# Optimization experiments

Measured on AMD Instinct MI355X. Metric: run time of the kernel, lower is better.

Reference implementation:

```python
import jax, jax.numpy as jnp
import numpy as np

C = 192; G = 12; CG = C // G          # channels, groups, channels per group
KS = 3; PAD = 1; K = KS * KS - 1      # 3x3 kernel, remove_center=True -> 8 points
HID = 4 * C                           # mlp_ratio = 4
OFFSET_SCALE = 1.0

# kernel dilation grid (x, y) pairs, center removed (remove_center=True)
_pts = np.arange(KS) - (KS - 1) // 2
_gx, _gy = np.meshgrid(_pts, _pts, indexing='ij')
_grid = np.stack([_gx.ravel(), _gy.ravel()], -1).astype(np.float32)
_grid = _grid[~np.all(_grid == 0, axis=1)]   # (K, 2)
GRID = jnp.asarray(_grid)


def _ln(x, w, b, eps=1e-5):
    mu = jnp.mean(x, -1, keepdims=True)
    var = jnp.var(x, -1, keepdims=True)
    return (x - mu) * jax.lax.rsqrt(var + eps) * w + b


def _dcnv3(x, in_proj_w, in_proj_b, dw_w, dw_b, dw_ln_w, dw_ln_b,
           off_w, off_b, mask_w, mask_b, cfs_w, cfs_b, out_proj_w, out_proj_b):
    # x: (B, H, W, C) channels-last
    B, H, W, _ = x.shape
    xp = x @ in_proj_w + in_proj_b          # value / x_proj
    # depthwise conv -> LN -> GELU on the raw input (offset/mask branch)
    x1 = jax.lax.conv_general_dilated(
        x, dw_w, (1, 1), 'SAME',
        dimension_numbers=('NHWC', 'HWIO', 'NHWC'),
        feature_group_count=C) + dw_b
    x1 = jax.nn.gelu(_ln(x1, dw_ln_w, dw_ln_b, 1e-6), approximate=False)
    off = (x1 @ off_w + off_b).reshape(B, H, W, G, K, 2)      # (dx, dy) in pixels
    mask = jax.nn.softmax((x1 @ mask_w + mask_b).reshape(B, H, W, G, K), axis=-1)
    # pad value and flatten spatial; (B, Hp*Wp, G, 1, CG)
    Hp, Wp = H + 2 * PAD, W + 2 * PAD
    v = jnp.pad(xp, ((0, 0), (PAD, PAD), (PAD, PAD), (0, 0))).reshape(B, Hp * Wp, G, 1, CG)
    # sampling locations in padded-image pixel index coords (grid_sample align_corners=False)
    bx = jnp.arange(W, dtype=x.dtype)[None, None, :, None, None] + PAD
    by = jnp.arange(H, dtype=x.dtype)[None, :, None, None, None] + PAD
    px = (bx + (GRID[:, 0] + off[..., 0]) * OFFSET_SCALE).reshape(B, H * W, G, K)
    py = (by + (GRID[:, 1] + off[..., 1]) * OFFSET_SCALE).reshape(B, H * W, G, K)
    x0 = jnp.floor(px); y0 = jnp.floor(py)
    wx = px - x0; wy = py - y0
    ix0 = x0.astype(jnp.int32); iy0 = y0.astype(jnp.int32)

    def gather(iy, ix):
        valid = ((iy >= 0) & (iy < Hp) & (ix >= 0) & (ix < Wp)).astype(x.dtype)
        idx = jnp.clip(iy, 0, Hp - 1) * Wp + jnp.clip(ix, 0, Wp - 1)
        s = jnp.take_along_axis(v, idx[..., None], axis=1)    # (B, HW, G, K, CG)
        return s * valid[..., None]

    s = (gather(iy0, ix0)         * ((1 - wy) * (1 - wx))[..., None]
       + gather(iy0, ix0 + 1)     * ((1 - wy) * wx)[..., None]
       + gather(iy0 + 1, ix0)     * (wy * (1 - wx))[..., None]
       + gather(iy0 + 1, ix0 + 1) * (wy * wx)[..., None])
    out = jnp.einsum('bngk,bngkc->bngc', mask.reshape(B, H * W, G, K), s).reshape(B, H, W, C)
    # center feature scale
    cfs = jax.nn.sigmoid(x1 @ cfs_w.T + cfs_b)                # (B, H, W, G)
    cfs = jnp.repeat(cfs, CG, axis=-1)                        # (B, H, W, C)
    out = out * (1 - cfs) + xp * cfs
    return out @ out_proj_w + out_proj_b


def _forward(x, norm1_w, norm1_b, norm2_w, norm2_b, rpn1_w, rpn1_b, rpn2_w, rpn2_b,
             in_proj_w, in_proj_b, dw_w, dw_b, dw_ln_w, dw_ln_b, off_w, off_b,
             mask_w, mask_b, cfs_w, cfs_b, out_proj_w, out_proj_b,
             fc1_w, fc1_b, fc2_w, fc2_b):
    d = _dcnv3(_ln(x, norm1_w, norm1_b), in_proj_w, in_proj_b, dw_w, dw_b,
               dw_ln_w, dw_ln_b, off_w, off_b, mask_w, mask_b, cfs_w, cfs_b,
               out_proj_w, out_proj_b)
    x = x + _ln(d, rpn1_w, rpn1_b)                            # res_post_norm branch 1
    h = jax.nn.gelu(_ln(x, norm2_w, norm2_b) @ fc1_w + fc1_b, approximate=False) @ fc2_w + fc2_b
    x = x + _ln(h, rpn2_w, rpn2_b)                            # res_post_norm branch 2
    return x


def setup_inputs():
    key = jax.random.key(0)
    ks = jax.random.split(key, 12)
    r = lambda i, shape, s=0.02: jax.random.normal(ks[i], shape, jnp.float32) * s
    B, H, W = 4, 56, 56
    return dict(
        x=jax.random.normal(ks[0], (B, H, W, C), jnp.float32),
        norm1_w=jnp.ones((C,)), norm1_b=jnp.zeros((C,)),
        norm2_w=jnp.ones((C,)), norm2_b=jnp.zeros((C,)),
        rpn1_w=jnp.ones((C,)), rpn1_b=jnp.zeros((C,)),
        rpn2_w=jnp.ones((C,)), rpn2_b=jnp.zeros((C,)),
        in_proj_w=r(1, (C, C)), in_proj_b=jnp.zeros((C,)),
        dw_w=r(2, (KS, KS, 1, C), 0.1), dw_b=jnp.zeros((C,)),
        dw_ln_w=jnp.ones((C,)), dw_ln_b=jnp.zeros((C,)),
        off_w=r(3, (C, G * K * 2), 0.1), off_b=jnp.zeros((G * K * 2,)),
        mask_w=r(4, (C, G * K), 0.1), mask_b=jnp.zeros((G * K,)),
        cfs_w=r(5, (G, C), 0.1), cfs_b=jnp.zeros((G,)),
        out_proj_w=r(6, (C, C)), out_proj_b=jnp.zeros((C,)),
        fc1_w=r(7, (C, HID)), fc1_b=jnp.zeros((HID,)),
        fc2_w=r(8, (HID, C)), fc2_b=jnp.zeros((C,)),
    )


def reference(x, norm1_w, norm1_b, norm2_w, norm2_b, rpn1_w, rpn1_b, rpn2_w, rpn2_b,
              in_proj_w, in_proj_b, dw_w, dw_b, dw_ln_w, dw_ln_b, off_w, off_b,
              mask_w, mask_b, cfs_w, cfs_b, out_proj_w, out_proj_b,
              fc1_w, fc1_b, fc2_w, fc2_b):
    return _forward(x, norm1_w, norm1_b, norm2_w, norm2_b, rpn1_w, rpn1_b, rpn2_w, rpn2_b,
                    in_proj_w, in_proj_b, dw_w, dw_b, dw_ln_w, dw_ln_b, off_w, off_b,
                    mask_w, mask_b, cfs_w, cfs_b, out_proj_w, out_proj_b,
                    fc1_w, fc1_b, fc2_w, fc2_b)
```

## Files before the change

### kernel.cpp

```cpp
#include <hip/hip_runtime.h>
#include <hip/hip_bf16.h>
#include <math.h>


#define BATCH 4
#define HH 56
#define WW 56
#define CC 192
#define NPIX (BATCH * HH * WW)
#define XS_STR 200
#define H1S 776
#define OFS 193
#define MLS 97

typedef __hip_bfloat16 bf16;
typedef __attribute__((ext_vector_type(8))) short short8;
typedef __attribute__((ext_vector_type(4))) float float4v;

__device__ __forceinline__ float gelu_exact(float x) {
    return 0.5f * x * (1.f + erff(x * 0.70710678118654752f));
}
__device__ __forceinline__ bf16 f2b(float f) { return __float2bfloat16(f); }
__device__ __forceinline__ float b2f(bf16 h) { return __bfloat162float(h); }
__device__ __forceinline__ float4 ldb4(const bf16* p) {
    const ushort4 u = *(const ushort4*)p;
    float4 r;
    r.x = __uint_as_float((unsigned)u.x << 16);
    r.y = __uint_as_float((unsigned)u.y << 16);
    r.z = __uint_as_float((unsigned)u.z << 16);
    r.w = __uint_as_float((unsigned)u.w << 16);
    return r;
}
__device__ __forceinline__ void stb4(bf16* p, float4 v) {
    ushort4 u;
    bf16 h;
    h = f2b(v.x); u.x = *(unsigned short*)&h;
    h = f2b(v.y); u.y = *(unsigned short*)&h;
    h = f2b(v.z); u.z = *(unsigned short*)&h;
    h = f2b(v.w); u.w = *(unsigned short*)&h;
    *(ushort4*)p = u;
}

__global__ __launch_bounds__(256) void ln4_k(const float* __restrict__ X,
        const float* __restrict__ w, const float* __restrict__ b,
        bf16* __restrict__ out, float eps)
{
    const int pix  = blockIdx.x * 4 + (threadIdx.x >> 6);
    const int lane = threadIdx.x & 63;
    const size_t base = (size_t)pix * CC;
    float v[3];
    #pragma unroll
    for (int i = 0; i < 3; i++) v[i] = X[base + lane + 64 * i];
    float s = v[0] + v[1] + v[2];
    float q = v[0]*v[0] + v[1]*v[1] + v[2]*v[2];
    #pragma unroll
    for (int off = 32; off > 0; off >>= 1) {
        s += __shfl_xor(s, off, 64);
        q += __shfl_xor(q, off, 64);
    }
    const float mu  = s * (1.f / CC);
    const float var = q * (1.f / CC) - mu * mu;
    const float rs  = rsqrtf(var + eps);
    #pragma unroll
    for (int i = 0; i < 3; i++) {
        const int c = lane + 64 * i;
        out[base + c] = f2b((v[i] - mu) * rs * w[c] + b[c]);
    }
}

__global__ __launch_bounds__(256) void dwconv_ln_gelu_k(
        const bf16* __restrict__ xn, const float* __restrict__ dww,
        const float* __restrict__ dwb, const float* __restrict__ lnw,
        const float* __restrict__ lnb, bf16* __restrict__ x1)
{
    __shared__ float cv[4][192];
    const int bid  = (blockIdx.x & 7) * (NPIX / 32) + (blockIdx.x >> 3);
    const int t    = threadIdx.x;
    const int ws   = t >> 6;
    const int l    = t & 63;
    const int pix  = bid * 4 + ws;
    const int bimg = pix / (HH * WW);
    const int hw   = pix - bimg * HH * WW;
    const int h    = hw / WW;
    const int wx   = hw - h * WW;

    if (l < 48) {
        const int c0 = l * 4;
        float4 acc = *(const float4*)&dwb[c0];
        #pragma unroll
        for (int ky = 0; ky < 3; ky++) {
            const int yy = h + ky - 1;
            if (yy < 0 || yy >= HH) continue;
            #pragma unroll
            for (int kx = 0; kx < 3; kx++) {
                const int xx = wx + kx - 1;
                if (xx < 0 || xx >= WW) continue;
                const float4 a = ldb4(&xn[((size_t)(bimg * HH + yy) * WW + xx) * CC + c0]);
                const float4 ww = *(const float4*)&dww[(ky * 3 + kx) * CC + c0];
                acc.x += a.x * ww.x; acc.y += a.y * ww.y;
                acc.z += a.z * ww.z; acc.w += a.w * ww.w;
            }
        }
        *(float4*)&cv[ws][c0] = acc;
    }
    __syncthreads();

    float v[3];
    #pragma unroll
    for (int i = 0; i < 3; i++) v[i] = cv[ws][l + 64 * i];
    float s = v[0] + v[1] + v[2];
    float q = v[0]*v[0] + v[1]*v[1] + v[2]*v[2];
    #pragma unroll
    for (int off = 32; off > 0; off >>= 1) {
        s += __shfl_xor(s, off, 64);
        q += __shfl_xor(q, off, 64);
    }
    const float mu  = s * (1.f / CC);
    const float var = q * (1.f / CC) - mu * mu;
    const float rs  = rsqrtf(var + 1e-6f);
    #pragma unroll
    for (int i = 0; i < 3; i++) {
        const int c = l + 64 * i;
        x1[(size_t)pix * CC + c] = f2b(gelu_exact((v[i] - mu) * rs * lnw[c] + lnb[c]));
    }
}

__global__ __launch_bounds__(256) void prep_w_k(const float* __restrict__ inpw,
        const float* __restrict__ offw, const float* __restrict__ maskw,
        const float* __restrict__ outpw, const float* __restrict__ fc1w,
        const float* __restrict__ fc2w, bf16* __restrict__ wsB)
{
    const int i = blockIdx.x * 256 + threadIdx.x;
    bf16* inpP = wsB;
    bf16* omP  = wsB + 36864;
    bf16* outP = wsB + 92160;
    bf16* fc1P = wsB + 129024;
    bf16* fc2P = wsB + 276480;
    const int j   = i & 7;
    const int l   = (i >> 3) & 63;
    const int n15 = l & 15, q = l >> 4;
    const int grp = i >> 9;
    if (i < 36864) {
        const int t = grp / 6, c = grp - t * 6;
        const int n = 16 * t + n15, k = 32 * c + 8 * q + j;
        inpP[i] = f2b(inpw[(size_t)k * 192 + n]);
        outP[i] = f2b(outpw[(size_t)k * 192 + n]);
    }
    if (i < 55296) {
        const int t = grp / 6, c = grp - t * 6;
        const int n = 16 * t + n15, k = 32 * c + 8 * q + j;
        omP[i] = (n < 192) ? f2b(offw[(size_t)k * 192 + n])
                           : f2b(maskw[(size_t)k * 96 + (n - 192)]);
    }
    if (i < 147456) {
        const int t1 = grp / 6, c1 = grp - t1 * 6;
        const int n1 = 16 * t1 + n15, k1 = 32 * c1 + 8 * q + j;
        fc1P[i] = f2b(fc1w[(size_t)k1 * 768 + n1]);
        const int t2 = grp / 24, c2 = grp - t2 * 24;
        const int n2 = 16 * t2 + n15, k2 = 32 * c2 + 8 * q + j;
        fc2P[i] = f2b(fc2w[(size_t)k2 * 192 + n2]);
    }
}

__global__ __launch_bounds__(256) void gemm16_k(const bf16* __restrict__ A,
        const bf16* __restrict__ wP, const float* __restrict__ bias,
        bf16* __restrict__ out)
{
    __shared__ __align__(16) bf16 xs[16 * XS_STR];
    const int tid = threadIdx.x;
    const int w   = tid >> 6;
    const int l   = tid & 63;
    const int n15 = l & 15;
    const int q   = l >> 4;
    const int p0  = blockIdx.x * 16;

    for (int i = tid; i < 16 * 24; i += 256) {
        const int px = i / 24, c8 = i - px * 24;
        *(short8*)&xs[px * XS_STR + c8 * 8] = *(const short8*)&A[(size_t)(p0 + px) * 192 + c8 * 8];
    }
    __syncthreads();

    short8 aF[6];
    #pragma unroll
    for (int c = 0; c < 6; c++)
        aF[c] = *(const short8*)&xs[n15 * XS_STR + c * 32 + q * 8];

    #pragma unroll
    for (int t = 0; t < 3; t++) {
        const int tile = 3 * w + t;
        float4v acc = (float4v){0.f, 0.f, 0.f, 0.f};
        #pragma unroll
        for (int c = 0; c < 6; c++) {
            const short8 bF = *(const short8*)&wP[(size_t)((tile * 6 + c) * 64 + l) * 8];
            acc = __builtin_amdgcn_mfma_f32_16x16x32_bf16(aF[c], bF, acc, 0, 0, 0);
        }
        const int n0 = 16 * tile;
        const float bb = bias[n0 + n15];
        #pragma unroll
        for (int r = 0; r < 4; r++)
            out[(size_t)(p0 + 4 * q + r) * 192 + n0 + n15] = f2b(acc[r] + bb);
    }
}

__global__ __launch_bounds__(256) void offmask_sample_k(
        const bf16* __restrict__ xp, const bf16* __restrict__ x1g,
        const bf16* __restrict__ omP, const float* __restrict__ offb,
        const float* __restrict__ maskb, const float* __restrict__ cfsw,
        const float* __restrict__ cfsb, bf16* __restrict__ outb)
{
    __shared__ __align__(16) bf16 xs[16 * XS_STR];
    __shared__ float offs_l[16][OFS];
    __shared__ float mls_l[16][MLS];

    const int tid = threadIdx.x;
    const int w   = tid >> 6;
    const int l   = tid & 63;
    const int n15 = l & 15;
    const int q   = l >> 4;
    const int bid = (blockIdx.x & 7) * (NPIX / 128) + (blockIdx.x >> 3);
    const int p0  = bid * 16;

    for (int i = tid; i < 16 * 24; i += 256) {
        const int px = i / 24, c8 = i - px * 24;
        *(short8*)&xs[px * XS_STR + c8 * 8] = *(const short8*)&x1g[(size_t)(p0 + px) * 192 + c8 * 8];
    }
    __syncthreads();

    {
        short8 aF[6];
        #pragma unroll
        for (int c = 0; c < 6; c++)
            aF[c] = *(const short8*)&xs[n15 * XS_STR + c * 32 + q * 8];

        for (int t = w; t < 18; t += 4) {
            float4v acc = (float4v){0.f, 0.f, 0.f, 0.f};
            #pragma unroll
            for (int c = 0; c < 6; c++) {
                const short8 bF = *(const short8*)&omP[(size_t)((t * 6 + c) * 64 + l) * 8];
                acc = __builtin_amdgcn_mfma_f32_16x16x32_bf16(aF[c], bF, acc, 0, 0, 0);
            }
            const int n0 = 16 * t;
            if (t < 12) {
                const float bb = offb[n0 + n15];
                #pragma unroll
                for (int r = 0; r < 4; r++)
                    offs_l[4 * q + r][n0 + n15] = acc[r] + bb;
            } else {
                const int m0 = n0 - 192;
                const float bb = maskb[m0 + n15];
                #pragma unroll
                for (int r = 0; r < 4; r++)
                    mls_l[4 * q + r][m0 + n15] = acc[r] + bb;
            }
        }
    }
    __syncthreads();

    #pragma unroll
    for (int it = 0; it < 3; it++) {
        const int id  = tid + 256 * it;
        const int px  = id / 48;
        const int s2  = id - px * 48;
        const int g   = s2 >> 2;
        const int c4  = s2 & 3;
        const int ch0 = g * 16 + c4 * 4;
        const int pix = p0 + px;
        const int bimg = pix / (HH * WW);
        const int hw   = pix - bimg * HH * WW;
        const int h    = hw / WW;
        const int wxp  = hw - h * WW;

        float lg[8];
        float mx = -1e30f;
        #pragma unroll
        for (int k = 0; k < 8; k++) { lg[k] = mls_l[px][g * 8 + k]; mx = fmaxf(mx, lg[k]); }
        float se = 0.f;
        #pragma unroll
        for (int k = 0; k < 8; k++) { lg[k] = expf(lg[k] - mx); se += lg[k]; }
        const float inv = 1.f / se;

        const int GX[8] = {-1, -1, -1, 0, 0, 1, 1, 1};
        const int GY[8] = {-1, 0, 1, -1, 1, -1, 0, 1};
        const size_t imgbase = (size_t)bimg * HH * WW * CC;

        float4 acc = {0.f, 0.f, 0.f, 0.f};
        #pragma unroll 2
        for (int k = 0; k < 8; k++) {
            const float px_ = (float)wxp + (float)GX[k] + offs_l[px][g * 16 + 2 * k];
            const float py_ = (float)h   + (float)GY[k] + offs_l[px][g * 16 + 2 * k + 1];
            const float fx = floorf(px_), fy = floorf(py_);
            const float wxf = px_ - fx, wyf = py_ - fy;
            const int x0 = (int)fx, y0 = (int)fy;
            float4 v00 = {0,0,0,0}, v01 = {0,0,0,0}, v10 = {0,0,0,0}, v11 = {0,0,0,0};
            if (y0 >= 0 && y0 < HH) {
                if (x0 >= 0 && x0 < WW)
                    v00 = ldb4(&xp[imgbase + (size_t)(y0 * WW + x0) * CC + ch0]);
                if (x0 + 1 >= 0 && x0 + 1 < WW)
                    v01 = ldb4(&xp[imgbase + (size_t)(y0 * WW + x0 + 1) * CC + ch0]);
            }
            if (y0 + 1 >= 0 && y0 + 1 < HH) {
                if (x0 >= 0 && x0 < WW)
                    v10 = ldb4(&xp[imgbase + (size_t)((y0 + 1) * WW + x0) * CC + ch0]);
                if (x0 + 1 >= 0 && x0 + 1 < WW)
                    v11 = ldb4(&xp[imgbase + (size_t)((y0 + 1) * WW + x0 + 1) * CC + ch0]);
            }
            const float w00 = (1.f - wyf) * (1.f - wxf), w01 = (1.f - wyf) * wxf;
            const float w10 = wyf * (1.f - wxf),         w11 = wyf * wxf;
            const float mk = lg[k] * inv;
            acc.x += mk * (w00 * v00.x + w01 * v01.x + w10 * v10.x + w11 * v11.x);
            acc.y += mk * (w00 * v00.y + w01 * v01.y + w10 * v10.y + w11 * v11.y);
            acc.z += mk * (w00 * v00.z + w01 * v01.z + w10 * v10.z + w11 * v11.z);
            acc.w += mk * (w00 * v00.w + w01 * v01.w + w10 * v10.w + w11 * v11.w);
        }

        float part = 0.f;
        #pragma unroll
        for (int j = 0; j < 48; j++)
            part += b2f(xs[px * XS_STR + 4 * j + c4]) * cfsw[(size_t)g * CC + 4 * j + c4];
        part += __shfl_xor(part, 1, 64);
        part += __shfl_xor(part, 2, 64);
        const float cf = 1.f / (1.f + expf(-(part + cfsb[g])));

        const float4 xpc = ldb4(&xp[(size_t)pix * CC + ch0]);
        float4 o;
        o.x = acc.x * (1.f - cf) + xpc.x * cf;
        o.y = acc.y * (1.f - cf) + xpc.y * cf;
        o.z = acc.z * (1.f - cf) + xpc.z * cf;
        o.w = acc.w * (1.f - cf) + xpc.w * cf;
        stb4(&outb[(size_t)pix * CC + ch0], o);
    }
}

__global__ __launch_bounds__(256) void gemm_ln2_mfma_k(const bf16* __restrict__ A,
        const bf16* __restrict__ wP, const float* __restrict__ bias,
        const float* __restrict__ x,
        const float* __restrict__ r1w, const float* __restrict__ r1b,
        const float* __restrict__ n2w, const float* __restrict__ n2b,
        float* __restrict__ x2out, bf16* __restrict__ xn2out)
{
    __shared__ __align__(16) bf16 xs[16 * XS_STR];
    __shared__ float ps[4][16], pq[4][16], ps2[4][16], pq2[4][16];
    const int tid = threadIdx.x;
    const int w   = tid >> 6;
    const int l   = tid & 63;
    const int n15 = l & 15;
    const int q   = l >> 4;
    const int p0  = blockIdx.x * 16;

    for (int i = tid; i < 16 * 24; i += 256) {
        const int px = i / 24, c8 = i - px * 24;
        *(short8*)&xs[px * XS_STR + c8 * 8] = *(const short8*)&A[(size_t)(p0 + px) * 192 + c8 * 8];
    }
    __syncthreads();

    short8 aF[6];
    #pragma unroll
    for (int c = 0; c < 6; c++)
        aF[c] = *(const short8*)&xs[n15 * XS_STR + c * 32 + q * 8];

    float4v acc[3];
    #pragma unroll
    for (int t = 0; t < 3; t++) {
        const int tile = 3 * w + t;
        acc[t] = (float4v){0.f, 0.f, 0.f, 0.f};
        #pragma unroll
        for (int c = 0; c < 6; c++) {
            const short8 bF = *(const short8*)&wP[(size_t)((tile * 6 + c) * 64 + l) * 8];
            acc[t] = __builtin_amdgcn_mfma_f32_16x16x32_bf16(aF[c], bF, acc[t], 0, 0, 0);
        }
        const float bb = bias[16 * tile + n15];
        #pragma unroll
        for (int r = 0; r < 4; r++) acc[t][r] += bb;
    }

    #pragma unroll
    for (int r = 0; r < 4; r++) {
        float sp = acc[0][r] + acc[1][r] + acc[2][r];
        float qp = acc[0][r]*acc[0][r] + acc[1][r]*acc[1][r] + acc[2][r]*acc[2][r];
        #pragma unroll
        for (int o = 1; o < 16; o <<= 1) {
            sp += __shfl_xor(sp, o, 64);
            qp += __shfl_xor(qp, o, 64);
        }
        if (n15 == 0) { ps[w][4 * q + r] = sp; pq[w][4 * q + r] = qp; }
    }
    __syncthreads();

    float x2v[3][4];
    #pragma unroll
    for (int r = 0; r < 4; r++) {
        const int row = 4 * q + r;
        const float s  = ps[0][row] + ps[1][row] + ps[2][row] + ps[3][row];
        const float qq = pq[0][row] + pq[1][row] + pq[2][row] + pq[3][row];
        const float mu  = s * (1.f / CC);
        const float var = qq * (1.f / CC) - mu * mu;
        const float rs  = rsqrtf(var + 1e-5f);
        const size_t grow = p0 + row;
        #pragma unroll
        for (int t = 0; t < 3; t++) {
            const int col = 48 * w + 16 * t + n15;
            x2v[t][r] = x[grow * CC + col] + (acc[t][r] - mu) * rs * r1w[col] + r1b[col];
        }
    }

    #pragma unroll
    for (int r = 0; r < 4; r++) {
        float sp = x2v[0][r] + x2v[1][r] + x2v[2][r];
        float qp = x2v[0][r]*x2v[0][r] + x2v[1][r]*x2v[1][r] + x2v[2][r]*x2v[2][r];
        #pragma unroll
        for (int o = 1; o < 16; o <<= 1) {
            sp += __shfl_xor(sp, o, 64);
            qp += __shfl_xor(qp, o, 64);
        }
        if (n15 == 0) { ps2[w][4 * q + r] = sp; pq2[w][4 * q + r] = qp; }
    }
    __syncthreads();

    #pragma unroll
    for (int r = 0; r < 4; r++) {
        const int row = 4 * q + r;
        const float s  = ps2[0][row] + ps2[1][row] + ps2[2][row] + ps2[3][row];
        const float qq = pq2[0][row] + pq2[1][row] + pq2[2][row] + pq2[3][row];
        const float mu  = s * (1.f / CC);
        const float var = qq * (1.f / CC) - mu * mu;
        const float rs  = rsqrtf(var + 1e-5f);
        const size_t grow = p0 + row;
        #pragma unroll
        for (int t = 0; t < 3; t++) {
            const int col = 48 * w + 16 * t + n15;
            x2out[grow * CC + col]  = x2v[t][r];
            xn2out[grow * CC + col] = f2b((x2v[t][r] - mu) * rs * n2w[col] + n2b[col]);
        }
    }
}

__global__ __launch_bounds__(256) void mlp_mfma16_k(const bf16* __restrict__ xn2,
        const bf16* __restrict__ fc1P, const float* __restrict__ fc1b,
        const bf16* __restrict__ fc2P, const float* __restrict__ fc2b,
        const float* __restrict__ x2, const float* __restrict__ r2w,
        const float* __restrict__ r2b, float* __restrict__ out)
{
    __shared__ __align__(16) bf16 xs[16 * XS_STR];
    __shared__ __align__(16) bf16 h1[16 * H1S];
    __shared__ float ps[4][16], pq[4][16];

    const int tid = threadIdx.x;
    const int w   = tid >> 6;
    const int l   = tid & 63;
    const int n15 = l & 15;
    const int q   = l >> 4;
    const int p0  = blockIdx.x * 16;

    for (int i = tid; i < 16 * 24; i += 256) {
        const int px = i / 24, c8 = i - px * 24;
        *(short8*)&xs[px * XS_STR + c8 * 8] = *(const short8*)&xn2[(size_t)(p0 + px) * 192 + c8 * 8];
    }
    __syncthreads();

    short8 aF[6];
    #pragma unroll
    for (int c = 0; c < 6; c++)
        aF[c] = *(const short8*)&xs[n15 * XS_STR + c * 32 + q * 8];

    #pragma unroll
    for (int t1 = 0; t1 < 12; t1++) {
        const int tile = 12 * w + t1;
        float4v a1 = (float4v){0.f, 0.f, 0.f, 0.f};
        #pragma unroll
        for (int c = 0; c < 6; c++) {
            const short8 bF = *(const short8*)&fc1P[(size_t)((tile * 6 + c) * 64 + l) * 8];
            a1 = __builtin_amdgcn_mfma_f32_16x16x32_bf16(aF[c], bF, a1, 0, 0, 0);
        }
        const int n0 = 16 * tile;
        const float bb = fc1b[n0 + n15];
        #pragma unroll
        for (int r = 0; r < 4; r++)
            h1[(4 * q + r) * H1S + n0 + n15] = f2b(gelu_exact(a1[r] + bb));
    }
    __syncthreads();

    float4v acc2[3];
    #pragma unroll
    for (int t = 0; t < 3; t++) acc2[t] = (float4v){0.f, 0.f, 0.f, 0.f};
    #pragma unroll 4
    for (int kc = 0; kc < 24; kc++) {
        const short8 a2 = *(const short8*)&h1[n15 * H1S + kc * 32 + q * 8];
        #pragma unroll
        for (int t = 0; t < 3; t++) {
            const int tile = 3 * w + t;
            const short8 bF = *(const short8*)&fc2P[(size_t)((tile * 24 + kc) * 64 + l) * 8];
            acc2[t] = __builtin_amdgcn_mfma_f32_16x16x32_bf16(a2, bF, acc2[t], 0, 0, 0);
        }
    }
    #pragma unroll
    for (int t = 0; t < 3; t++) {
        const float bb = fc2b[48 * w + 16 * t + n15];
        #pragma unroll
        for (int r = 0; r < 4; r++) acc2[t][r] += bb;
    }

    #pragma unroll
    for (int r = 0; r < 4; r++) {
        float sp = acc2[0][r] + acc2[1][r] + acc2[2][r];
        float qp = acc2[0][r]*acc2[0][r] + acc2[1][r]*acc2[1][r] + acc2[2][r]*acc2[2][r];
        #pragma unroll
        for (int o = 1; o < 16; o <<= 1) {
            sp += __shfl_xor(sp, o, 64);
            qp += __shfl_xor(qp, o, 64);
        }
        if (n15 == 0) { ps[w][4 * q + r] = sp; pq[w][4 * q + r] = qp; }
    }
    __syncthreads();

    #pragma unroll
    for (int r = 0; r < 4; r++) {
        const int row = 4 * q + r;
        const float s  = ps[0][row] + ps[1][row] + ps[2][row] + ps[3][row];
        const float qq = pq[0][row] + pq[1][row] + pq[2][row] + pq[3][row];
        const float mu  = s * (1.f / CC);
        const float var = qq * (1.f / CC) - mu * mu;
        const float rs  = rsqrtf(var + 1e-5f);
        const size_t grow = p0 + row;
        #pragma unroll
        for (int t = 0; t < 3; t++) {
            const int col = 48 * w + 16 * t + n15;
            out[grow * CC + col] = x2[grow * CC + col]
                                 + (acc2[t][r] - mu) * rs * r2w[col] + r2b[col];
        }
    }
}

extern "C" void kernel_launch(void* const* d_in, const int* in_sizes, int n_in,
                              void* d_out, int out_size, void* d_ws, size_t ws_size,
                              hipStream_t stream) {
    const float* x      = (const float*)d_in[0];
    const float* n1w    = (const float*)d_in[1];
    const float* n1b    = (const float*)d_in[2];
    const float* n2w    = (const float*)d_in[3];
    const float* n2b    = (const float*)d_in[4];
    const float* rpn1w  = (const float*)d_in[5];
    const float* rpn1b  = (const float*)d_in[6];
    const float* rpn2w  = (const float*)d_in[7];
    const float* rpn2b  = (const float*)d_in[8];
    const float* inpw   = (const float*)d_in[9];
    const float* inpb   = (const float*)d_in[10];
    const float* dww    = (const float*)d_in[11];
    const float* dwb    = (const float*)d_in[12];
    const float* dwlnw  = (const float*)d_in[13];
    const float* dwlnb  = (const float*)d_in[14];
    const float* offw   = (const float*)d_in[15];
    const float* offb   = (const float*)d_in[16];
    const float* maskw  = (const float*)d_in[17];
    const float* maskb  = (const float*)d_in[18];
    const float* cfsw   = (const float*)d_in[19];
    const float* cfsb   = (const float*)d_in[20];
    const float* outpw  = (const float*)d_in[21];
    const float* outpb  = (const float*)d_in[22];
    const float* fc1w   = (const float*)d_in[23];
    const float* fc1b   = (const float*)d_in[24];
    const float* fc2w   = (const float*)d_in[25];
    const float* fc2b   = (const float*)d_in[26];

    const int N = NPIX;
    const size_t NP = (size_t)N * CC;
    bf16*  B0  = (bf16*)d_ws;
    bf16*  B1  = B0 + NP;
    bf16*  B3  = B1 + NP;
    float* Fx2 = (float*)(B3 + NP);
    bf16*  wsB = (bf16*)(Fx2 + NP);
    const bf16* inpP = wsB;
    const bf16* omP  = wsB + 36864;
    const bf16* outP = wsB + 92160;
    const bf16* fc1P = wsB + 129024;
    const bf16* fc2P = wsB + 276480;

    const int lnG = N / 4;
    const int g16 = N / 16;

    prep_w_k<<<576, 256, 0, stream>>>(inpw, offw, maskw, outpw, fc1w, fc2w, wsB);
    ln4_k<<<lnG, 256, 0, stream>>>(x, n1w, n1b, B0, 1e-5f);
    gemm16_k<<<g16, 256, 0, stream>>>(B0, inpP, inpb, B1);
    dwconv_ln_gelu_k<<<lnG, 256, 0, stream>>>(B0, dww, dwb, dwlnw, dwlnb, B3);
    offmask_sample_k<<<g16, 256, 0, stream>>>(B1, B3, omP, offb, maskb,
                                              cfsw, cfsb, B0);
    gemm_ln2_mfma_k<<<g16, 256, 0, stream>>>(B0, outP, outpb, x, rpn1w, rpn1b,
                                             n2w, n2b, Fx2, B3);
    mlp_mfma16_k<<<g16, 256, 0, stream>>>(B3, fc1P, fc1b, fc2P, fc2b,
                                          Fx2, rpn2w, rpn2b, (float*)d_out);
}
```

Measured before the change: 219.1 us.

## Fuse LN1 into input projection GEMM and out-proj/LN2 into MLP kernel

Folds the first LayerNorm into the input-projection GEMM kernel, which now writes both the normalized input and the projection. It also merges the output projection, residual and LN2 kernel with the MLP kernel, keeping x2 in registers and the LN2 output in shared memory. This drops two launches and the global round trips for the fp32 x2 buffer and the bf16 LN2 output. The fused MLP kernel uses more shared memory and registers per block, which may lower occupancy.

```diff
diff --git a/kernel.cpp b/kernel.cpp
--- a/kernel.cpp
+++ b/kernel.cpp
@@ -39,90 +39,6 @@
     h = f2b(v.z); u.z = *(unsigned short*)&h;
     h = f2b(v.w); u.w = *(unsigned short*)&h;
     *(ushort4*)p = u;
-}
-
-__global__ __launch_bounds__(256) void ln4_k(const float* __restrict__ X,
-        const float* __restrict__ w, const float* __restrict__ b,
-        bf16* __restrict__ out, float eps)
-{
-    const int pix  = blockIdx.x * 4 + (threadIdx.x >> 6);
-    const int lane = threadIdx.x & 63;
-    const size_t base = (size_t)pix * CC;
-    float v[3];
-    #pragma unroll
-    for (int i = 0; i < 3; i++) v[i] = X[base + lane + 64 * i];
-    float s = v[0] + v[1] + v[2];
-    float q = v[0]*v[0] + v[1]*v[1] + v[2]*v[2];
-    #pragma unroll
-    for (int off = 32; off > 0; off >>= 1) {
-        s += __shfl_xor(s, off, 64);
-        q += __shfl_xor(q, off, 64);
-    }
-    const float mu  = s * (1.f / CC);
-    const float var = q * (1.f / CC) - mu * mu;
-    const float rs  = rsqrtf(var + eps);
-    #pragma unroll
-    for (int i = 0; i < 3; i++) {
-        const int c = lane + 64 * i;
-        out[base + c] = f2b((v[i] - mu) * rs * w[c] + b[c]);
-    }
-}
-
-__global__ __launch_bounds__(256) void dwconv_ln_gelu_k(
-        const bf16* __restrict__ xn, const float* __restrict__ dww,
-        const float* __restrict__ dwb, const float* __restrict__ lnw,
-        const float* __restrict__ lnb, bf16* __restrict__ x1)
-{
-    __shared__ float cv[4][192];
-    const int bid  = (blockIdx.x & 7) * (NPIX / 32) + (blockIdx.x >> 3);
-    const int t    = threadIdx.x;
-    const int ws   = t >> 6;
-    const int l    = t & 63;
-    const int pix  = bid * 4 + ws;
-    const int bimg = pix / (HH * WW);
-    const int hw   = pix - bimg * HH * WW;
-    const int h    = hw / WW;
-    const int wx   = hw - h * WW;
-
-    if (l < 48) {
-        const int c0 = l * 4;
-        float4 acc = *(const float4*)&dwb[c0];
-        #pragma unroll
-        for (int ky = 0; ky < 3; ky++) {
-            const int yy = h + ky - 1;
-            if (yy < 0 || yy >= HH) continue;
-            #pragma unroll
-            for (int kx = 0; kx < 3; kx++) {
-                const int xx = wx + kx - 1;
-                if (xx < 0 || xx >= WW) continue;
-                const float4 a = ldb4(&xn[((size_t)(bimg * HH + yy) * WW + xx) * CC + c0]);
-                const float4 ww = *(const float4*)&dww[(ky * 3 + kx) * CC + c0];
-                acc.x += a.x * ww.x; acc.y += a.y * ww.y;
-                acc.z += a.z * ww.z; acc.w += a.w * ww.w;
-            }
-        }
-        *(float4*)&cv[ws][c0] = acc;
-    }
-    __syncthreads();
-
-    float v[3];
-    #pragma unroll
-    for (int i = 0; i < 3; i++) v[i] = cv[ws][l + 64 * i];
-    float s = v[0] + v[1] + v[2];
-    float q = v[0]*v[0] + v[1]*v[1] + v[2]*v[2];
-    #pragma unroll
-    for (int off = 32; off > 0; off >>= 1) {
-        s += __shfl_xor(s, off, 64);
-        q += __shfl_xor(q, off, 64);
-    }
-    const float mu  = s * (1.f / CC);
-    const float var = q * (1.f / CC) - mu * mu;
-    const float rs  = rsqrtf(var + 1e-6f);
-    #pragma unroll
-    for (int i = 0; i < 3; i++) {
-        const int c = l + 64 * i;
-        x1[(size_t)pix * CC + c] = f2b(gelu_exact((v[i] - mu) * rs * lnw[c] + lnb[c]));
-    }
 }
 
 __global__ __launch_bounds__(256) void prep_w_k(const float* __restrict__ inpw,
@@ -162,9 +78,10 @@
     }
 }
 
-__global__ __launch_bounds__(256) void gemm16_k(const bf16* __restrict__ A,
+__global__ __launch_bounds__(256) void ln_gemm16_k(const float* __restrict__ x,
+        const float* __restrict__ n1w, const float* __restrict__ n1b,
         const bf16* __restrict__ wP, const float* __restrict__ bias,
-        bf16* __restrict__ out)
+        bf16* __restrict__ xn_out, bf16* __restrict__ xp_out)
 {
     __shared__ __align__(16) bf16 xs[16 * XS_STR];
     const int tid = threadIdx.x;
@@ -174,9 +91,30 @@
     const int q   = l >> 4;
     const int p0  = blockIdx.x * 16;
 
-    for (int i = tid; i < 16 * 24; i += 256) {
-        const int px = i / 24, c8 = i - px * 24;
-        *(short8*)&xs[px * XS_STR + c8 * 8] = *(const short8*)&A[(size_t)(p0 + px) * 192 + c8 * 8];
+    #pragma unroll
+    for (int rr = 0; rr < 4; rr++) {
+        const int lr = 4 * w + rr;
+        const size_t base = (size_t)(p0 + lr) * CC;
+        float v[3];
+        #pragma unroll
+        for (int i = 0; i < 3; i++) v[i] = x[base + l + 64 * i];
+        float s = v[0] + v[1] + v[2];
+        float qq = v[0]*v[0] + v[1]*v[1] + v[2]*v[2];
+        #pragma unroll
+        for (int off = 32; off > 0; off >>= 1) {
+            s  += __shfl_xor(s, off, 64);
+            qq += __shfl_xor(qq, off, 64);
+        }
+        const float mu  = s * (1.f / CC);
+        const float var = qq * (1.f / CC) - mu * mu;
+        const float rs  = rsqrtf(var + 1e-5f);
+        #pragma unroll
+        for (int i = 0; i < 3; i++) {
+            const int c = l + 64 * i;
+            const bf16 h = f2b((v[i] - mu) * rs * n1w[c] + n1b[c]);
+            xs[lr * XS_STR + c] = h;
+            xn_out[base + c] = h;
+        }
     }
     __syncthreads();
 
@@ -198,7 +136,64 @@
         const float bb = bias[n0 + n15];
         #pragma unroll
         for (int r = 0; r < 4; r++)
-            out[(size_t)(p0 + 4 * q + r) * 192 + n0 + n15] = f2b(acc[r] + bb);
+            xp_out[(size_t)(p0 + 4 * q + r) * 192 + n0 + n15] = f2b(acc[r] + bb);
+    }
+}
+
+__global__ __launch_bounds__(256) void dwconv_ln_gelu_k(
+        const bf16* __restrict__ xn, const float* __restrict__ dww,
+        const float* __restrict__ dwb, const float* __restrict__ lnw,
+        const float* __restrict__ lnb, bf16* __restrict__ x1)
+{
+    __shared__ float cv[4][192];
+    const int bid  = (blockIdx.x & 7) * (NPIX / 32) + (blockIdx.x >> 3);
+    const int t    = threadIdx.x;
+    const int ws   = t >> 6;
+    const int l    = t & 63;
+    const int pix  = bid * 4 + ws;
+    const int bimg = pix / (HH * WW);
+    const int hw   = pix - bimg * HH * WW;
+    const int h    = hw / WW;
+    const int wx   = hw - h * WW;
+
+    if (l < 48) {
+        const int c0 = l * 4;
+        float4 acc = *(const float4*)&dwb[c0];
+        #pragma unroll
+        for (int ky = 0; ky < 3; ky++) {
+            const int yy = h + ky - 1;
+            if (yy < 0 || yy >= HH) continue;
+            #pragma unroll
+            for (int kx = 0; kx < 3; kx++) {
+                const int xx = wx + kx - 1;
+                if (xx < 0 || xx >= WW) continue;
+                const float4 a = ldb4(&xn[((size_t)(bimg * HH + yy) * WW + xx) * CC + c0]);
+                const float4 ww = *(const float4*)&dww[(ky * 3 + kx) * CC + c0];
+                acc.x += a.x * ww.x; acc.y += a.y * ww.y;
+                acc.z += a.z * ww.z; acc.w += a.w * ww.w;
+            }
+        }
+        *(float4*)&cv[ws][c0] = acc;
+    }
+    __syncthreads();
+
+    float v[3];
+    #pragma unroll
+    for (int i = 0; i < 3; i++) v[i] = cv[ws][l + 64 * i];
+    float s = v[0] + v[1] + v[2];
+    float q = v[0]*v[0] + v[1]*v[1] + v[2]*v[2];
+    #pragma unroll
+    for (int off = 32; off > 0; off >>= 1) {
+        s += __shfl_xor(s, off, 64);
+        q += __shfl_xor(q, off, 64);
+    }
+    const float mu  = s * (1.f / CC);
+    const float var = q * (1.f / CC) - mu * mu;
+    const float rs  = rsqrtf(var + 1e-6f);
+    #pragma unroll
+    for (int i = 0; i < 3; i++) {
+        const int c = l + 64 * i;
+        x1[(size_t)pix * CC + c] = f2b(gelu_exact((v[i] - mu) * rs * lnw[c] + lnb[c]));
     }
 }
 
@@ -331,15 +326,20 @@
     }
 }
 
-__global__ __launch_bounds__(256) void gemm_ln2_mfma_k(const bf16* __restrict__ A,
+__global__ __launch_bounds__(256) void gemm_ln2_mlp_k(const bf16* __restrict__ A,
         const bf16* __restrict__ wP, const float* __restrict__ bias,
         const float* __restrict__ x,
         const float* __restrict__ r1w, const float* __restrict__ r1b,
         const float* __restrict__ n2w, const float* __restrict__ n2b,
-        float* __restrict__ x2out, bf16* __restrict__ xn2out)
+        const bf16* __restrict__ fc1P, const float* __restrict__ fc1b,
+        const bf16* __restrict__ fc2P, const float* __restrict__ fc2b,
+        const float* __restrict__ r2w, const float* __restrict__ r2b,
+        float* __restrict__ out)
 {
     __shared__ __align__(16) bf16 xs[16 * XS_STR];
+    __shared__ __align__(16) bf16 h1[16 * H1S];
     __shared__ float ps[4][16], pq[4][16], ps2[4][16], pq2[4][16];
+
     const int tid = threadIdx.x;
     const int w   = tid >> 6;
     const int l   = tid & 63;
@@ -353,179 +353,155 @@
     }
     __syncthreads();
 
-    short8 aF[6];
-    #pragma unroll
-    for (int c = 0; c < 6; c++)
-        aF[c] = *(const short8*)&xs[n15 * XS_STR + c * 32 + q * 8];
-
-    float4v acc[3];
-    #pragma unroll
-    for (int t = 0; t < 3; t++) {
-        const int tile = 3 * w + t;
-        acc[t] = (float4v){0.f, 0.f, 0.f, 0.f};
-        #pragma unroll
-        for (int c = 0; c < 6; c++) {
-            const short8 bF = *(const short8*)&wP[(size_t)((tile * 6 + c) * 64 + l) * 8];
-            acc[t] = __builtin_amdgcn_mfma_f32_16x16x32_bf16(aF[c], bF, acc[t], 0, 0, 0);
-        }
-        const float bb = bias[16 * tile + n15];
-        #pragma unroll
-        for (int r = 0; r < 4; r++) acc[t][r] += bb;
-    }
-
-    #pragma unroll
-    for (int r = 0; r < 4; r++) {
-        float sp = acc[0][r] + acc[1][r] + acc[2][r];
-        float qp = acc[0][r]*acc[0][r] + acc[1][r]*acc[1][r] + acc[2][r]*acc[2][r];
-        #pragma unroll
-        for (int o = 1; o < 16; o <<= 1) {
-            sp += __shfl_xor(sp, o, 64);
-            qp += __shfl_xor(qp, o, 64);
-        }
-        if (n15 == 0) { ps[w][4 * q + r] = sp; pq[w][4 * q + r] = qp; }
-    }
-    __syncthreads();
-
-    float x2v[3][4];
-    #pragma unroll
-    for (int r = 0; r < 4; r++) {
-        const int row = 4 * q + r;
-        const float s  = ps[0][row] + ps[1][row] + ps[2][row] + ps[3][row];
-        const float qq = pq[0][row] + pq[1][row] + pq[2][row] + pq[3][row];
-        const float mu  = s * (1.f / CC);
-        const float var = qq * (1.f / CC) - mu * mu;
-        const float rs  = rsqrtf(var + 1e-5f);
-        const size_t grow = p0 + row;
-        #pragma unroll
-        for (int t = 0; t < 3; t++) {
-            const int col = 48 * w + 16 * t + n15;
-            x2v[t][r] = x[grow * CC + col] + (acc[t][r] - mu) * rs * r1w[col] + r1b[col];
-        }
-    }
-
-    #pragma unroll
-    for (int r = 0; r < 4; r++) {
-        float sp = x2v[0][r] + x2v[1][r] + x2v[2][r];
-        float qp = x2v[0][r]*x2v[0][r] + x2v[1][r]*x2v[1][r] + x2v[2][r]*x2v[2][r];
-        #pragma unroll
-        for (int o = 1; o < 16; o <<= 1) {
-            sp += __shfl_xor(sp, o, 64);
-            qp += __shfl_xor(qp, o, 64);
-        }
-        if (n15 == 0) { ps2[w][4 * q + r] = sp; pq2[w][4 * q + r] = qp; }
-    }
-    __syncthreads();
-
-    #pragma unroll
-    for (int r = 0; r < 4; r++) {
-        const int row = 4 * q + r;
-        const float s  = ps2[0][row] + ps2[1][row] + ps2[2][row] + ps2[3][row];
-        const float qq = pq2[0][row] + pq2[1][row] + pq2[2][row] + pq2[3][row];
-        const float mu  = s * (1.f / CC);
-        const float var = qq * (1.f / CC) - mu * mu;
-        const float rs  = rsqrtf(var + 1e-5f);
-        const size_t grow = p0 + row;
-        #pragma unroll
-        for (int t = 0; t < 3; t++) {
-            const int col = 48 * w + 16 * t + n15;
-            x2out[grow * CC + col]  = x2v[t][r];
-            xn2out[grow * CC + col] = f2b((x2v[t][r] - mu) * rs * n2w[col] + n2b[col]);
-        }
-    }
-}
-
-__global__ __launch_bounds__(256) void mlp_mfma16_k(const bf16* __restrict__ xn2,
-        const bf16* __restrict__ fc1P, const float* __restrict__ fc1b,
-        const bf16* __restrict__ fc2P, const float* __restrict__ fc2b,
-        const float* __restrict__ x2, const float* __restrict__ r2w,
-        const float* __restrict__ r2b, float* __restrict__ out)
-{
-    __shared__ __align__(16) bf16 xs[16 * XS_STR];
-    __shared__ __align__(16) bf16 h1[16 * H1S];
-    __shared__ float ps[4][16], pq[4][16];
-
-    const int tid = threadIdx.x;
-    const int w   = tid >> 6;
-    const int l   = tid & 63;
-    const int n15 = l & 15;
-    const int q   = l >> 4;
-    const int p0  = blockIdx.x * 16;
-
-    for (int i = tid; i < 16 * 24; i += 256) {
-        const int px = i / 24, c8 = i - px * 24;
-        *(short8*)&xs[px * XS_STR + c8 * 8] = *(const short8*)&xn2[(size_t)(p0 + px) * 192 + c8 * 8];
-    }
-    __syncthreads();
-
-    short8 aF[6];
-    #pragma unroll
-    for (int c = 0; c < 6; c++)
-        aF[c] = *(const short8*)&xs[n15 * XS_STR + c * 32 + q * 8];
-
-    #pragma unroll
-    for (int t1 = 0; t1 < 12; t1++) {
-        const int tile = 12 * w + t1;
-        float4v a1 = (float4v){0.f, 0.f, 0.f, 0.f};
-        #pragma unroll
-        for (int c = 0; c < 6; c++) {
-            const short8 bF = *(const short8*)&fc1P[(size_t)((tile * 6 + c) * 64 + l) * 8];
-            a1 = __builtin_amdgcn_mfma_f32_16x16x32_bf16(aF[c], bF, a1, 0, 0, 0);
-        }
-        const int n0 = 16 * tile;
-        const float bb = fc1b[n0 + n15];
-        #pragma unroll
-        for (int r = 0; r < 4; r++)
-            h1[(4 * q + r) * H1S + n0 + n15] = f2b(gelu_exact(a1[r] + bb));
-    }
-    __syncthreads();
-
-    float4v acc2[3];
-    #pragma unroll
-    for (int t = 0; t < 3; t++) acc2[t] = (float4v){0.f, 0.f, 0.f, 0.f};
-    #pragma unroll 4
-    for (int kc = 0; kc < 24; kc++) {
-        const short8 a2 = *(const short8*)&h1[n15 * H1S + kc * 32 + q * 8];
+    {
+        short8 aF[6];
+        #pragma unroll
+        for (int c = 0; c < 6; c++)
+            aF[c] = *(const short8*)&xs[n15 * XS_STR + c * 32 + q * 8];
+
+        float4v acc[3];
         #pragma unroll
         for (int t = 0; t < 3; t++) {
             const int tile = 3 * w + t;
-            const short8 bF = *(const short8*)&fc2P[(size_t)((tile * 24 + kc) * 64 + l) * 8];
-            acc2[t] = __builtin_amdgcn_mfma_f32_16x16x32_bf16(a2, bF, acc2[t], 0, 0, 0);
-        }
-    }
-    #pragma unroll
-    for (int t = 0; t < 3; t++) {
-        const float bb = fc2b[48 * w + 16 * t + n15];
-        #pragma unroll
-        for (int r = 0; r < 4; r++) acc2[t][r] += bb;
-    }
-
-    #pragma unroll
-    for (int r = 0; r < 4; r++) {
-        float sp = acc2[0][r] + acc2[1][r] + acc2[2][r];
-        float qp = acc2[0][r]*acc2[0][r] + acc2[1][r]*acc2[1][r] + acc2[2][r]*acc2[2][r];
-        #pragma unroll
-        for (int o = 1; o < 16; o <<= 1) {
-            sp += __shfl_xor(sp, o, 64);
-            qp += __shfl_xor(qp, o, 64);
-        }
-        if (n15 == 0) { ps[w][4 * q + r] = sp; pq[w][4 * q + r] = qp; }
-    }
-    __syncthreads();
-
-    #pragma unroll
-    for (int r = 0; r < 4; r++) {
-        const int row = 4 * q + r;
-        const float s  = ps[0][row] + ps[1][row] + ps[2][row] + ps[3][row];
-        const float qq = pq[0][row] + pq[1][row] + pq[2][row] + pq[3][row];
-        const float mu  = s * (1.f / CC);
-        const float var = qq * (1.f / CC) - mu * mu;
-        const float rs  = rsqrtf(var + 1e-5f);
-        const size_t grow = p0 + row;
+            acc[t] = (float4v){0.f, 0.f, 0.f, 0.f};
+            #pragma unroll
+            for (int c = 0; c < 6; c++) {
+                const short8 bF = *(const short8*)&wP[(size_t)((tile * 6 + c) * 64 + l) * 8];
+                acc[t] = __builtin_amdgcn_mfma_f32_16x16x32_bf16(aF[c], bF, acc[t], 0, 0, 0);
+            }
+            const float bb = bias[16 * tile + n15];
+            #pragma unroll
+            for (int r = 0; r < 4; r++) acc[t][r] += bb;
+        }
+
+        #pragma unroll
+        for (int r = 0; r < 4; r++) {
+            float sp = acc[0][r] + acc[1][r] + acc[2][r];
+            float qp = acc[0][r]*acc[0][r] + acc[1][r]*acc[1][r] + acc[2][r]*acc[2][r];
+            #pragma unroll
+            for (int o = 1; o < 16; o <<= 1) {
+                sp += __shfl_xor(sp, o, 64);
+                qp += __shfl_xor(qp, o, 64);
+            }
+            if (n15 == 0) { ps[w][4 * q + r] = sp; pq[w][4 * q + r] = qp; }
+        }
+        __syncthreads();
+
+        float x2v[3][4];
+        #pragma unroll
+        for (int r = 0; r < 4; r++) {
+            const int row = 4 * q + r;
+            const float s  = ps[0][row] + ps[1][row] + ps[2][row] + ps[3][row];
+            const float qq = pq[0][row] + pq[1][row] + pq[2][row] + pq[3][row];
+            const float mu  = s * (1.f / CC);
+            const float var = qq * (1.f / CC) - mu * mu;
+            const float rs  = rsqrtf(var + 1e-5f);
+            const size_t grow = p0 + row;
+            #pragma unroll
+            for (int t = 0; t < 3; t++) {
+                const int col = 48 * w + 16 * t + n15;
+                x2v[t][r] = x[grow * CC + col] + (acc[t][r] - mu) * rs * r1w[col] + r1b[col];
+            }
+        }
+        #pragma unroll
+        for (int r = 0; r < 4; r++) {
+            float sp = x2v[0][r] + x2v[1][r] + x2v[2][r];
+            float qp = x2v[0][r]*x2v[0][r] + x2v[1][r]*x2v[1][r] + x2v[2][r]*x2v[2][r];
+            #pragma unroll
+            for (int o = 1; o < 16; o <<= 1) {
+                sp += __shfl_xor(sp, o, 64);
+                qp += __shfl_xor(qp, o, 64);
+            }
+            if (n15 == 0) { ps2[w][4 * q + r] = sp; pq2[w][4 * q + r] = qp; }
+        }
+        __syncthreads();
+
+        #pragma unroll
+        for (int r = 0; r < 4; r++) {
+            const int row = 4 * q + r;
+            const float s  = ps2[0][row] + ps2[1][row] + ps2[2][row] + ps2[3][row];
+            const float qq = pq2[0][row] + pq2[1][row] + pq2[2][row] + pq2[3][row];
+            const float mu  = s * (1.f / CC);
+            const float var = qq * (1.f / CC) - mu * mu;
+            const float rs  = rsqrtf(var + 1e-5f);
+            #pragma unroll
+            for (int t = 0; t < 3; t++) {
+                const int col = 48 * w + 16 * t + n15;
+                xs[row * XS_STR + col] = f2b((x2v[t][r] - mu) * rs * n2w[col] + n2b[col]);
+            }
+        }
+        __syncthreads();
+
+        short8 aF2[6];
+        #pragma unroll
+        for (int c = 0; c < 6; c++)
+            aF2[c] = *(const short8*)&xs[n15 * XS_STR + c * 32 + q * 8];
+
+        #pragma unroll
+        for (int t1 = 0; t1 < 12; t1++) {
+            const int tile = 12 * w + t1;
+            float4v a1 = (float4v){0.f, 0.f, 0.f, 0.f};
+            #pragma unroll
+            for (int c = 0; c < 6; c++) {
+                const short8 bF = *(const short8*)&fc1P[(size_t)((tile * 6 + c) * 64 + l) * 8];
+                a1 = __builtin_amdgcn_mfma_f32_16x16x32_bf16(aF2[c], bF, a1, 0, 0, 0);
+            }
+            const int n0 = 16 * tile;
+            const float bb = fc1b[n0 + n15];
+            #pragma unroll
+            for (int r = 0; r < 4; r++)
+                h1[(4 * q + r) * H1S + n0 + n15] = f2b(gelu_exact(a1[r] + bb));
+        }
+        __syncthreads();
+
+        float4v acc2[3];
+        #pragma unroll
+        for (int t = 0; t < 3; t++) acc2[t] = (float4v){0.f, 0.f, 0.f, 0.f};
+        #pragma unroll 4
+        for (int kc = 0; kc < 24; kc++) {
+            const short8 a2 = *(const short8*)&h1[n15 * H1S + kc * 32 + q * 8];
+            #pragma unroll
+            for (int t = 0; t < 3; t++) {
+                const int tile = 3 * w + t;
+                const short8 bF = *(const short8*)&fc2P[(size_t)((tile * 24 + kc) * 64 + l) * 8];
+                acc2[t] = __builtin_amdgcn_mfma_f32_16x16x32_bf16(a2, bF, acc2[t], 0, 0, 0);
+            }
+        }
         #pragma unroll
         for (int t = 0; t < 3; t++) {
-            const int col = 48 * w + 16 * t + n15;
-            out[grow * CC + col] = x2[grow * CC + col]
-                                 + (acc2[t][r] - mu) * rs * r2w[col] + r2b[col];
+            const float bb = fc2b[48 * w + 16 * t + n15];
+            #pragma unroll
+            for (int r = 0; r < 4; r++) acc2[t][r] += bb;
+        }
+
+        #pragma unroll
+        for (int r = 0; r < 4; r++) {
+            float sp = acc2[0][r] + acc2[1][r] + acc2[2][r];
+            float qp = acc2[0][r]*acc2[0][r] + acc2[1][r]*acc2[1][r] + acc2[2][r]*acc2[2][r];
+            #pragma unroll
+            for (int o = 1; o < 16; o <<= 1) {
+                sp += __shfl_xor(sp, o, 64);
+                qp += __shfl_xor(qp, o, 64);
+            }
+            if (n15 == 0) { ps[w][4 * q + r] = sp; pq[w][4 * q + r] = qp; }
+        }
+        __syncthreads();
+
+        #pragma unroll
+        for (int r = 0; r < 4; r++) {
+            const int row = 4 * q + r;
+            const float s  = ps[0][row] + ps[1][row] + ps[2][row] + ps[3][row];
+            const float qq = pq[0][row] + pq[1][row] + pq[2][row] + pq[3][row];
+            const float mu  = s * (1.f / CC);
+            const float var = qq * (1.f / CC) - mu * mu;
+            const float rs  = rsqrtf(var + 1e-5f);
+            const size_t grow = p0 + row;
+            #pragma unroll
+            for (int t = 0; t < 3; t++) {
+                const int col = 48 * w + 16 * t + n15;
+                out[grow * CC + col] = x2v[t][r]
+                                     + (acc2[t][r] - mu) * rs * r2w[col] + r2b[col];
+            }
         }
     }
 }
@@ -563,11 +539,10 @@
 
     const int N = NPIX;
     const size_t NP = (size_t)N * CC;
-    bf16*  B0  = (bf16*)d_ws;
-    bf16*  B1  = B0 + NP;
-    bf16*  B3  = B1 + NP;
-    float* Fx2 = (float*)(B3 + NP);
-    bf16*  wsB = (bf16*)(Fx2 + NP);
+    bf16* B0  = (bf16*)d_ws;
+    bf16* B1  = B0 + NP;
+    bf16* B3  = B1 + NP;
+    bf16* wsB = B3 + NP;
     const bf16* inpP = wsB;
     const bf16* omP  = wsB + 36864;
     const bf16* outP = wsB + 92160;
@@ -578,13 +553,11 @@
     const int g16 = N / 16;
 
     prep_w_k<<<576, 256, 0, stream>>>(inpw, offw, maskw, outpw, fc1w, fc2w, wsB);
-    ln4_k<<<lnG, 256, 0, stream>>>(x, n1w, n1b, B0, 1e-5f);
-    gemm16_k<<<g16, 256, 0, stream>>>(B0, inpP, inpb, B1);
+    ln_gemm16_k<<<g16, 256, 0, stream>>>(x, n1w, n1b, inpP, inpb, B0, B1);
     dwconv_ln_gelu_k<<<lnG, 256, 0, stream>>>(B0, dww, dwb, dwlnw, dwlnb, B3);
     offmask_sample_k<<<g16, 256, 0, stream>>>(B1, B3, omP, offb, maskb,
                                               cfsw, cfsb, B0);
-    gemm_ln2_mfma_k<<<g16, 256, 0, stream>>>(B0, outP, outpb, x, rpn1w, rpn1b,
-                                             n2w, n2b, Fx2, B3);
-    mlp_mfma16_k<<<g16, 256, 0, stream>>>(B3, fc1P, fc1b, fc2P, fc2b,
-                                          Fx2, rpn2w, rpn2b, (float*)d_out);
-}
+    gemm_ln2_mlp_k<<<g16, 256, 0, stream>>>(B0, outP, outpb, x, rpn1w, rpn1b,
+                                            n2w, n2b, fc1P, fc1b, fc2P, fc2b,
+                                            rpn2w, rpn2b, (float*)d_out);
+}
```

Measured after the change: 210.2 us. 1.04x faster.
